# Performance work log

Hardware: AMD Instinct MI355X
Metric: run time of the kernel (lower is better)

The kernel has to match this reference:

```python
import jax, jax.numpy as jnp
import numpy as np

D_MODEL = 1024
NUM_HEADS = 16
HEAD_DIM = D_MODEL // NUM_HEADS


def setup_inputs() -> dict:
    key = jax.random.key(0)
    k_x, k_qkv, k_proj, k_pb = jax.random.split(key, 4)
    x = jax.random.normal(k_x, (4, 2048, D_MODEL), dtype=jnp.float32)
    s = 1.0 / np.sqrt(D_MODEL)
    W_qkv = jax.random.uniform(k_qkv, (D_MODEL, 3 * D_MODEL), minval=-s, maxval=s, dtype=jnp.float32)
    W_proj = jax.random.uniform(k_proj, (D_MODEL, D_MODEL), minval=-s, maxval=s, dtype=jnp.float32)
    b_proj = jax.random.uniform(k_pb, (D_MODEL,), minval=-s, maxval=s, dtype=jnp.float32)
    return {"x": x, "W_qkv": W_qkv, "W_proj": W_proj, "b_proj": b_proj}


def reference(x, W_qkv, W_proj, b_proj):
    B, N, D = x.shape
    H, Hd = NUM_HEADS, HEAD_DIM
    scale = Hd ** -0.5
    qkv = jnp.einsum('bnd,de->bne', x, W_qkv)  # (B, N, 3D), no bias (qkv_bias=False)
    qkv = qkv.reshape(B, N, 3, H, Hd).transpose(2, 0, 3, 1, 4)  # (3, B, H, N, Hd)
    q, k, v = qkv[0], qkv[1], qkv[2]
    attn = jnp.einsum('bhqd,bhkd->bhqk', q, k) * scale  # (B, H, N, N)
    attn = jax.nn.softmax(attn, axis=-1)
    out = jnp.einsum('bhqk,bhkd->bhqd', attn, v)  # (B, H, N, Hd)
    out = out.transpose(0, 2, 1, 3).reshape(B, N, D)
    return jnp.einsum('bnd,de->bne', out, W_proj) + b_proj
```

## Files before the change

kernel.cpp:

```cpp
#include <hip/hip_runtime.h>


#define DEV __device__ __forceinline__

typedef __attribute__((ext_vector_type(8))) short bf16x8;
typedef __attribute__((ext_vector_type(4))) float f32x4;
typedef __attribute__((ext_vector_type(2))) __bf16 bf16x2v;

DEV unsigned short f2b(float f) {
  union { float f; unsigned u; } x; x.f = f;
  unsigned r = (x.u + 0x7FFFu + ((x.u >> 16) & 1u)) >> 16;
  return (unsigned short)r;
}

DEV unsigned pkbf(float a, float b) {
  bf16x2v v; v[0] = (__bf16)a; v[1] = (__bf16)b;
  union { bf16x2v v; unsigned u; } x; x.v = v; return x.u;
}

DEV void gload16(const void* g, void* l) {
  __builtin_amdgcn_global_load_lds((const __attribute__((address_space(1))) void*)g,
                                   (__attribute__((address_space(3))) void*)l,
                                   16, 0, 0);
}

__global__ void k_cvt(const float* __restrict__ in, unsigned short* __restrict__ out) {
  int i = (blockIdx.x * 256 + threadIdx.x) * 4;
  float4 v = *(const float4*)&in[i];
  *(uint2*)&out[i] = make_uint2(pkbf(v.x, v.y), pkbf(v.z, v.w));
}

__global__ void k_wt(const float* __restrict__ W, unsigned short* __restrict__ Wt,
                     int Nw, int K) {
  __shared__ float t[64][65];
  const int k0 = blockIdx.y * 64, n0 = blockIdx.x * 64;
  const int tx = threadIdx.x, ty = threadIdx.y;
#pragma unroll
  for (int i = 0; i < 16; ++i) {
    int r = i * 4 + ty;
    t[r][tx] = W[(size_t)(k0 + r) * Nw + n0 + tx];
  }
  __syncthreads();
#pragma unroll
  for (int i = 0; i < 16; ++i) {
    int r = i * 4 + ty;
    Wt[(size_t)(n0 + r) * K + k0 + tx] = f2b(t[tx][r]);
  }
}

__global__ void k_vt(const unsigned short* __restrict__ qkv, unsigned short* __restrict__ vt) {
  __shared__ unsigned short t[64][68];
  const int bh = blockIdx.y;
  const int b = bh >> 4, h = bh & 15;
  const int n0 = blockIdx.x * 64;
  const int tx = threadIdx.x, ty = threadIdx.y;
#pragma unroll
  for (int i = 0; i < 16; ++i) {
    int r = i * 4 + ty;
    t[r][tx] = qkv[(size_t)(b * 2048 + n0 + r) * 3072 + 2048 + h * 64 + tx];
  }
  __syncthreads();
#pragma unroll
  for (int i = 0; i < 16; ++i) {
    int d = i * 4 + ty;
    vt[(size_t)(bh * 64 + d) * 2048 + n0 + tx] = t[tx][d];
  }
}

template <bool PROJ>
__global__ __launch_bounds__(256, 2) void gemm_bt(
    const unsigned short* __restrict__ A, const unsigned short* __restrict__ Bt,
    unsigned short* __restrict__ outB, float* __restrict__ outF,
    const float* __restrict__ bias, int M, int N, int K) {
  __shared__ unsigned short Al[128 * 32];
  __shared__ unsigned short Bl[128 * 32];
  const int tid = threadIdx.x;
  const int lane = tid & 63;
  const int wv = tid >> 6;
  const int m0 = blockIdx.y * 128;
  const int n0 = blockIdx.x * 128;
  const int wrow = (wv >> 1) * 64;
  const int wcol = (wv & 1) * 64;

  f32x4 acc[4][4];
#pragma unroll
  for (int i = 0; i < 4; ++i)
#pragma unroll
    for (int j = 0; j < 4; ++j) acc[i][j] = (f32x4){0.f, 0.f, 0.f, 0.f};

  const int lr = lane >> 2;
  const int lk = (lane & 3) * 8;
  const int fr = lane & 15;
  const int fg = (lane >> 4) * 8;

  const unsigned short* gA = A + (size_t)(m0 + wv * 32 + lr) * K + lk;
  const unsigned short* gB = Bt + (size_t)(n0 + wv * 32 + lr) * K + lk;
  unsigned short* lA0 = &Al[(wv * 2 + 0) * 512];
  unsigned short* lA1 = &Al[(wv * 2 + 1) * 512];
  unsigned short* lB0 = &Bl[(wv * 2 + 0) * 512];
  unsigned short* lB1 = &Bl[(wv * 2 + 1) * 512];

  const int nk = K >> 5;
  for (int kt = 0; kt < nk; ++kt) {
    const int k0 = kt << 5;
    gload16(gA + k0, lA0);
    gload16(gA + k0 + (size_t)16 * K, lA1);
    gload16(gB + k0, lB0);
    gload16(gB + k0 + (size_t)16 * K, lB1);
    __syncthreads();
    bf16x8 af[4], bfv[4];
#pragma unroll
    for (int i = 0; i < 4; ++i) af[i] = *(const bf16x8*)&Al[(wrow + i * 16 + fr) * 32 + fg];
#pragma unroll
    for (int j = 0; j < 4; ++j) bfv[j] = *(const bf16x8*)&Bl[(wcol + j * 16 + fr) * 32 + fg];
#pragma unroll
    for (int i = 0; i < 4; ++i)
#pragma unroll
      for (int j = 0; j < 4; ++j)
        acc[i][j] = __builtin_amdgcn_mfma_f32_16x16x32_bf16(af[i], bfv[j], acc[i][j], 0, 0, 0);
    __syncthreads();
  }

  const int rg = (lane >> 4) * 4;
#pragma unroll
  for (int i = 0; i < 4; ++i) {
#pragma unroll
    for (int j = 0; j < 4; ++j) {
      const int col = n0 + wcol + j * 16 + fr;
#pragma unroll
      for (int r = 0; r < 4; ++r) {
        const int row = m0 + wrow + i * 16 + rg + r;
        if (PROJ)
          outF[(size_t)row * N + col] = acc[i][j][r] + bias[col];
        else
          outB[(size_t)row * N + col] = f2b(acc[i][j][r]);
      }
    }
  }
}

__global__ __launch_bounds__(256, 3) void attn_k(
    const unsigned short* __restrict__ qkv, const unsigned short* __restrict__ vt,
    unsigned short* __restrict__ ao) {
  __shared__ unsigned short Kl[2][64 * 64];
  __shared__ unsigned short Vl[2][64 * 64];
  __shared__ unsigned short Pl[4][32 * 72];
  const int tid = threadIdx.x;
  const int lane = tid & 63;
  const int wv = tid >> 6;
  const int id = blockIdx.x;
  const int swz = (id & 7) * (1024 >> 3) + (id >> 3);
  const int bh = swz >> 4;
  const int b = bh >> 4, h = bh & 15;
  const int q0 = (swz & 15) * 128 + wv * 32;
  const int fr = lane & 15;
  const int hi = lane >> 4;
  const int g8 = hi * 8;
  const int g4 = hi * 4;
  const int fx = fr & 7;
  const float CSC = 0.125f * 1.44269504f;
  const float THR = 4.0f;

  const int sr = lane >> 3;
  const int sc = ((lane & 7) ^ (sr & 7)) * 8;
  const unsigned short* gK =
      qkv + (size_t)(b * 2048 + wv * 16 + sr) * 3072 + 1024 + h * 64 + sc;
  const unsigned short* gV =
      vt + ((size_t)bh * 64 + wv * 16 + sr) * 2048 + sc;

  bf16x8 bq[2][2];
#pragma unroll
  for (int qt = 0; qt < 2; ++qt)
#pragma unroll
    for (int ks = 0; ks < 2; ++ks)
      bq[qt][ks] = *(const bf16x8*)&qkv[(size_t)(b * 2048 + q0 + qt * 16 + fr) * 3072 +
                                        h * 64 + ks * 32 + g8];

  bf16x8 vones;
#pragma unroll
  for (int j = 0; j < 8; ++j) vones[j] = (short)0x3F80;

  f32x4 acc[4][2];
  f32x4 acc_l[2];
#pragma unroll
  for (int i = 0; i < 4; ++i)
#pragma unroll
    for (int j = 0; j < 2; ++j) acc[i][j] = (f32x4){0.f, 0.f, 0.f, 0.f};
  acc_l[0] = (f32x4){0.f, 0.f, 0.f, 0.f};
  acc_l[1] = (f32x4){0.f, 0.f, 0.f, 0.f};
  float m[2] = {-1e30f, -1e30f};

  auto STAGE = [&](int buf, int tt) {
#pragma unroll
    for (int seg = 0; seg < 2; ++seg) {
      gload16(gK + (size_t)(tt * 64 + seg * 8) * 3072, &Kl[buf][(wv * 16 + seg * 8) * 64]);
      gload16(gV + (size_t)(seg * 8) * 2048 + tt * 64, &Vl[buf][(wv * 16 + seg * 8) * 64]);
    }
  };

  int cur = 0;
  STAGE(0, 0);
  __syncthreads();

  const f32x4 csc4 = (f32x4){CSC, CSC, CSC, CSC};

  for (int tt = 0; tt < 32; ++tt) {
    if (tt < 31) STAGE(cur ^ 1, tt + 1);
    const unsigned short* Kb = &Kl[cur][0];
    const unsigned short* Vb = &Vl[cur][0];

    f32x4 st[4][2];
    __builtin_amdgcn_s_setprio(1);
#pragma unroll
    for (int kk = 0; kk < 4; ++kk) {
      bf16x8 ak0 = *(const bf16x8*)&Kb[(kk * 16 + fr) * 64 + ((hi ^ fx) * 8)];
      bf16x8 ak1 = *(const bf16x8*)&Kb[(kk * 16 + fr) * 64 + (((4 + hi) ^ fx) * 8)];
#pragma unroll
      for (int qt = 0; qt < 2; ++qt) {
        f32x4 z = (f32x4){0.f, 0.f, 0.f, 0.f};
        z = __builtin_amdgcn_mfma_f32_16x16x32_bf16(ak0, bq[qt][0], z, 0, 0, 0);
        st[kk][qt] = __builtin_amdgcn_mfma_f32_16x16x32_bf16(ak1, bq[qt][1], z, 0, 0, 0);
      }
    }
    __builtin_amdgcn_s_setprio(0);

    f32x4 t0 = __builtin_elementwise_max(st[0][0], st[1][0]);
    t0 = __builtin_elementwise_max(t0, st[2][0]);
    t0 = __builtin_elementwise_max(t0, st[3][0]);
    f32x4 t1 = __builtin_elementwise_max(st[0][1], st[1][1]);
    t1 = __builtin_elementwise_max(t1, st[2][1]);
    t1 = __builtin_elementwise_max(t1, st[3][1]);
    const float c0 = fmaxf(fmaxf(t0[0], t0[1]), fmaxf(t0[2], t0[3])) * CSC;
    const float c1 = fmaxf(fmaxf(t1[0], t1[1]), fmaxf(t1[2], t1[3])) * CSC;

    if (!__all(c0 <= m[0] + THR && c1 <= m[1] + THR)) {
      const float cc[2] = {c0, c1};
#pragma unroll
      for (int qt = 0; qt < 2; ++qt) {
        float tm = cc[qt];
        tm = fmaxf(tm, __shfl_xor(tm, 16, 64));
        tm = fmaxf(tm, __shfl_xor(tm, 32, 64));
        const float mnew = fmaxf(m[qt], tm);
        const float corr = exp2f(m[qt] - mnew);
        m[qt] = mnew;
        acc_l[qt][0] *= corr;
#pragma unroll
        for (int dt = 0; dt < 4; ++dt) acc[dt][qt] *= corr;
      }
    }

#pragma unroll
    for (int qt = 0; qt < 2; ++qt) {
      const float mq = m[qt];
      const f32x4 mq4 = (f32x4){-mq, -mq, -mq, -mq};
      const int prow = (qt * 16 + fr) * 72;
#pragma unroll
      for (int kk = 0; kk < 4; ++kk) {
        f32x4 e = __builtin_elementwise_fma(st[kk][qt], csc4, mq4);
        *(uint2*)&Pl[wv][prow + kk * 16 + g4] =
            make_uint2(pkbf(exp2f(e[0]), exp2f(e[1])), pkbf(exp2f(e[2]), exp2f(e[3])));
      }
    }

#pragma unroll
    for (int ks2 = 0; ks2 < 2; ++ks2) {
      bf16x8 bp0 = *(const bf16x8*)&Pl[wv][(0 * 16 + fr) * 72 + ks2 * 32 + g8];
      bf16x8 bp1 = *(const bf16x8*)&Pl[wv][(1 * 16 + fr) * 72 + ks2 * 32 + g8];
      __builtin_amdgcn_s_setprio(1);
#pragma unroll
      for (int dt = 0; dt < 4; ++dt) {
        bf16x8 av = *(const bf16x8*)&Vb[(dt * 16 + fr) * 64 + (((ks2 * 4 + hi) ^ fx) * 8)];
        acc[dt][0] = __builtin_amdgcn_mfma_f32_16x16x32_bf16(av, bp0, acc[dt][0], 0, 0, 0);
        acc[dt][1] = __builtin_amdgcn_mfma_f32_16x16x32_bf16(av, bp1, acc[dt][1], 0, 0, 0);
      }
      acc_l[0] = __builtin_amdgcn_mfma_f32_16x16x32_bf16(vones, bp0, acc_l[0], 0, 0, 0);
      acc_l[1] = __builtin_amdgcn_mfma_f32_16x16x32_bf16(vones, bp1, acc_l[1], 0, 0, 0);
      __builtin_amdgcn_s_setprio(0);
    }

    __syncthreads();
    cur ^= 1;
  }

#pragma unroll
  for (int qt = 0; qt < 2; ++qt) {
    const float inv = 1.0f / acc_l[qt][0];
#pragma unroll
    for (int dt = 0; dt < 4; ++dt) {
      uint2 o = make_uint2(pkbf(acc[dt][qt][0] * inv, acc[dt][qt][1] * inv),
                           pkbf(acc[dt][qt][2] * inv, acc[dt][qt][3] * inv));
      *(uint2*)&ao[(size_t)(b * 2048 + q0 + qt * 16 + fr) * 1024 + h * 64 + dt * 16 + g4] = o;
    }
  }
}

extern "C" void kernel_launch(void* const* d_in, const int* in_sizes, int n_in,
                              void* d_out, int out_size, void* d_ws, size_t ws_size,
                              hipStream_t stream) {
  const float* x     = (const float*)d_in[0];
  const float* wqkv  = (const float*)d_in[1];
  const float* wproj = (const float*)d_in[2];
  const float* bproj = (const float*)d_in[3];
  float* out = (float*)d_out;
  char* ws = (char*)d_ws;

  unsigned short* xb     = (unsigned short*)(ws + 0);
  unsigned short* wqkvT  = (unsigned short*)(ws + 16777216);
  unsigned short* wprojT = (unsigned short*)(ws + 23068672);
  unsigned short* qkv    = (unsigned short*)(ws + 25165824);
  unsigned short* vt     = (unsigned short*)(ws + 75497472);
  unsigned short* ao     = (unsigned short*)(ws + 92274688);

  k_cvt<<<8192, 256, 0, stream>>>(x, xb);
  k_wt<<<dim3(48, 16), dim3(64, 4), 0, stream>>>(wqkv, wqkvT, 3072, 1024);
  k_wt<<<dim3(16, 16), dim3(64, 4), 0, stream>>>(wproj, wprojT, 1024, 1024);
  gemm_bt<false><<<dim3(24, 64), 256, 0, stream>>>(xb, wqkvT, qkv, nullptr, nullptr,
                                                   8192, 3072, 1024);
  k_vt<<<dim3(32, 64), dim3(64, 4), 0, stream>>>(qkv, vt);
  attn_k<<<1024, 256, 0, stream>>>(qkv, vt, ao);
  gemm_bt<true><<<dim3(8, 64), 256, 0, stream>>>(ao, wprojT, nullptr, out, bproj,
                                                 8192, 1024, 1024);
}
```

Measured before the change: 321.0 us.

## Double-buffer GEMM LDS tiles and use native exp2 in attention softmax

```diff
diff --git a/kernel.cpp b/kernel.cpp
--- a/kernel.cpp
+++ b/kernel.cpp
@@ -17,6 +17,12 @@
   bf16x2v v; v[0] = (__bf16)a; v[1] = (__bf16)b;
   union { bf16x2v v; unsigned u; } x; x.v = v; return x.u;
 }
+
+#if __has_builtin(__builtin_amdgcn_exp2f)
+DEV float fexp2(float x) { return __builtin_amdgcn_exp2f(x); }
+#else
+DEV float fexp2(float x) { return __exp2f(x); }
+#endif
 
 DEV void gload16(const void* g, void* l) {
   __builtin_amdgcn_global_load_lds((const __attribute__((address_space(1))) void*)g,
@@ -72,8 +78,8 @@
     const unsigned short* __restrict__ A, const unsigned short* __restrict__ Bt,
     unsigned short* __restrict__ outB, float* __restrict__ outF,
     const float* __restrict__ bias, int M, int N, int K) {
-  __shared__ unsigned short Al[128 * 32];
-  __shared__ unsigned short Bl[128 * 32];
+  __shared__ unsigned short Al[2][128 * 32];
+  __shared__ unsigned short Bl[2][128 * 32];
   const int tid = threadIdx.x;
   const int lane = tid & 63;
   const int wv = tid >> 6;
@@ -95,30 +101,37 @@
 
   const unsigned short* gA = A + (size_t)(m0 + wv * 32 + lr) * K + lk;
   const unsigned short* gB = Bt + (size_t)(n0 + wv * 32 + lr) * K + lk;
-  unsigned short* lA0 = &Al[(wv * 2 + 0) * 512];
-  unsigned short* lA1 = &Al[(wv * 2 + 1) * 512];
-  unsigned short* lB0 = &Bl[(wv * 2 + 0) * 512];
-  unsigned short* lB1 = &Bl[(wv * 2 + 1) * 512];
+
+  auto STAGE = [&](int buf, int kt) {
+    const size_t k0 = (size_t)kt << 5;
+    unsigned short* a = &Al[buf][(wv * 2) * 512];
+    unsigned short* b = &Bl[buf][(wv * 2) * 512];
+    gload16(gA + k0, a);
+    gload16(gA + k0 + (size_t)16 * K, a + 512);
+    gload16(gB + k0, b);
+    gload16(gB + k0 + (size_t)16 * K, b + 512);
+  };
 
   const int nk = K >> 5;
+  STAGE(0, 0);
   for (int kt = 0; kt < nk; ++kt) {
-    const int k0 = kt << 5;
-    gload16(gA + k0, lA0);
-    gload16(gA + k0 + (size_t)16 * K, lA1);
-    gload16(gB + k0, lB0);
-    gload16(gB + k0 + (size_t)16 * K, lB1);
+    const int cur = kt & 1;
     __syncthreads();
+    if (kt + 1 < nk) STAGE(cur ^ 1, kt + 1);
+    const unsigned short* Ab = &Al[cur][0];
+    const unsigned short* Bb = &Bl[cur][0];
     bf16x8 af[4], bfv[4];
 #pragma unroll
-    for (int i = 0; i < 4; ++i) af[i] = *(const bf16x8*)&Al[(wrow + i * 16 + fr) * 32 + fg];
-#pragma unroll
-    for (int j = 0; j < 4; ++j) bfv[j] = *(const bf16x8*)&Bl[(wcol + j * 16 + fr) * 32 + fg];
+    for (int i = 0; i < 4; ++i) af[i] = *(const bf16x8*)&Ab[(wrow + i * 16 + fr) * 32 + fg];
+#pragma unroll
+    for (int j = 0; j < 4; ++j) bfv[j] = *(const bf16x8*)&Bb[(wcol + j * 16 + fr) * 32 + fg];
+    __builtin_amdgcn_s_setprio(1);
 #pragma unroll
     for (int i = 0; i < 4; ++i)
 #pragma unroll
       for (int j = 0; j < 4; ++j)
         acc[i][j] = __builtin_amdgcn_mfma_f32_16x16x32_bf16(af[i], bfv[j], acc[i][j], 0, 0, 0);
-    __syncthreads();
+    __builtin_amdgcn_s_setprio(0);
   }
 
   const int rg = (lane >> 4) * 4;
@@ -241,7 +254,7 @@
         tm = fmaxf(tm, __shfl_xor(tm, 16, 64));
         tm = fmaxf(tm, __shfl_xor(tm, 32, 64));
         const float mnew = fmaxf(m[qt], tm);
-        const float corr = exp2f(m[qt] - mnew);
+        const float corr = fexp2(m[qt] - mnew);
         m[qt] = mnew;
         acc_l[qt][0] *= corr;
 #pragma unroll
@@ -258,7 +271,7 @@
       for (int kk = 0; kk < 4; ++kk) {
         f32x4 e = __builtin_elementwise_fma(st[kk][qt], csc4, mq4);
         *(uint2*)&Pl[wv][prow + kk * 16 + g4] =
-            make_uint2(pkbf(exp2f(e[0]), exp2f(e[1])), pkbf(exp2f(e[2]), exp2f(e[3])));
+            make_uint2(pkbf(fexp2(e[0]), fexp2(e[1])), pkbf(fexp2(e[2]), fexp2(e[3])));
       }
     }
 
```

Result: faster. 295.0 us (-8.1%).
